# Performance work log

Measured on AMD Instinct MI355X. Metric: run time of the kernel, lower is better.

## Reference

```python
import jax, jax.numpy as jnp
import numpy as np

B, N, T, D, H = 4, 8, 512, 256, 8
DK = D // H


def _dwconv(x, w, b=None):
    # x: (BN, D, T) depthwise conv, kernel 3, padding 'same', groups=D
    y = jax.lax.conv_general_dilated(
        x, w, window_strides=(1,), padding='SAME',
        feature_group_count=x.shape[1],
        dimension_numbers=('NCH', 'OIH', 'NCH'))
    if b is not None:
        y = y + b[None, :, None]
    return y


def setup_inputs() -> dict:
    key = jax.random.key(0)
    ks = jax.random.split(key, 16)
    s = 1.0 / np.sqrt(D)
    s3 = 1.0 / np.sqrt(3 * D)
    inp = {
        'query': jax.random.normal(ks[0], (B, N, T, D), jnp.float32),
        'key': jax.random.normal(ks[1], (B, N, T, D), jnp.float32),
        'value': jax.random.normal(ks[2], (B, N, T, D), jnp.float32),
        'key_padding_mask': jax.random.randint(ks[3], (B, N, T), 0, 2, jnp.int32),
        # depthwise conv params
        'w_pos': jax.random.uniform(ks[4], (D, 1, 3), jnp.float32, -0.577, 0.577),
        'b_pos': jax.random.uniform(ks[5], (D,), jnp.float32, -0.577, 0.577),
        # physics-initialized differential operators (still learnable floats)
        'w_vel': jnp.tile(jnp.array([-1.0, 0.0, 1.0], jnp.float32)[None, None, :], (D, 1, 1)),
        'w_acc': jnp.tile(jnp.array([1.0, -2.0, 1.0], jnp.float32)[None, None, :], (D, 1, 1)),
        # fusion / projection linears (stored as (in, out))
        'Wq': jax.random.uniform(ks[6], (3 * D, D), jnp.float32, -s3, s3),
        'bq': jax.random.uniform(ks[7], (D,), jnp.float32, -s3, s3),
        'Wk': jax.random.uniform(ks[8], (3 * D, D), jnp.float32, -s3, s3),
        'bk': jax.random.uniform(ks[9], (D,), jnp.float32, -s3, s3),
        'Wv': jax.random.uniform(ks[10], (D, D), jnp.float32, -s, s),
        'bv': jax.random.uniform(ks[11], (D,), jnp.float32, -s, s),
        'Wo': jax.random.uniform(ks[12], (D, D), jnp.float32, -s, s),
        'bo': jax.random.uniform(ks[13], (D,), jnp.float32, -s, s),
    }
    return inp


def reference(query, key, value, key_padding_mask,
              w_pos, b_pos, w_vel, w_acc,
              Wq, bq, Wk, bk, Wv, bv, Wo, bo):
    b, n, t, d = query.shape
    scale = jnp.float32(1.0 / np.sqrt(DK))

    def kin_feats(x):
        xin = x.reshape(b * n, t, d).transpose(0, 2, 1)  # (BN, D, T)
        p = _dwconv(xin, w_pos, b_pos)
        v = _dwconv(xin, w_vel)
        a = _dwconv(xin, w_acc)
        return jnp.concatenate([p, v, a], axis=1).transpose(0, 2, 1)  # (BN, T, 3D)

    qc = kin_feats(query)
    kc = kin_feats(key)

    Q = (qc @ Wq + bq).reshape(b, n, t, H, DK).transpose(0, 1, 3, 2, 4)  # (B,N,H,Tq,dk)
    K = (kc @ Wk + bk).reshape(b, n, t, H, DK).transpose(0, 1, 3, 2, 4)
    V = (value @ Wv + bv).reshape(b, n, t, H, DK).transpose(0, 1, 3, 2, 4)

    scores = jnp.einsum('bnhqd,bnhkd->bnhqk', Q, K) * scale
    mask = key_padding_mask.astype(bool)[:, :, None, None, :]  # (B,N,1,1,Tk)
    scores = jnp.where(mask, jnp.float32(-1e9), scores)
    attn = jax.nn.softmax(scores, axis=-1)  # dropout is identity in eval

    ctx = jnp.einsum('bnhqk,bnhkd->bnhqd', attn, V)
    ctx = ctx.transpose(0, 1, 3, 2, 4).reshape(b, n, t, d)
    return ctx @ Wo + bo
```

## Files before the change

kernel.cpp:

```cpp
#include <hip/hip_runtime.h>
#include <math.h>


typedef __attribute__((ext_vector_type(8))) short bf16x8;
typedef __attribute__((ext_vector_type(4))) float f32x4;
typedef __attribute__((ext_vector_type(16))) float f32x16;
typedef __attribute__((ext_vector_type(4))) int i32x4;

__device__ __forceinline__ unsigned short f2bf(float f) {
    unsigned u = __float_as_uint(f);
    return (unsigned short)((u + 0x7fff + ((u >> 16) & 1)) >> 16);
}
__device__ __forceinline__ float bf2f(unsigned short h) {
    return __uint_as_float(((unsigned)h) << 16);
}
__device__ __forceinline__ float ex2(float x) {
    float r; asm("v_exp_f32 %0, %1" : "=v"(r) : "v"(x)); return r;
}
__device__ __forceinline__ int cvtpk(float lo, float hi) {
    int r; asm("v_cvt_pk_bf16_f32 %0, %1, %2" : "=v"(r) : "v"(lo), "v"(hi)); return r;
}
__device__ __forceinline__ void gll16(const void* gsrc, const void* ldst) {
    __builtin_amdgcn_global_load_lds(
        (const __attribute__((address_space(1))) unsigned int*)gsrc,
        (__attribute__((address_space(3))) unsigned int*)ldst, 16, 0, 0);
}

#define SCL (0.17677669529663689f * 1.4426950408889634f)

#define OFF_XPQ  0u
#define OFF_XPK  8421376u
#define OFF_VB   16842752u
#define OFF_BTQ  25231360u
#define OFF_BTK  25624576u
#define OFF_BEFF 26017792u
#define OFF_WVT  26019840u
#define OFF_WOT  26150912u
#define OFF_QB   26413056u
#define OFF_KB   34801664u
#define OFF_VV   43190272u
#define OFF_CTX  51578880u

__global__ __launch_bounds__(256) void cvtprep(
    const float* __restrict__ q, const float* __restrict__ k, const float* __restrict__ v,
    unsigned short* __restrict__ xpq, unsigned short* __restrict__ xpk,
    unsigned short* __restrict__ vb,
    const float* __restrict__ Wq, const float* __restrict__ Wk,
    const float* __restrict__ bq, const float* __restrict__ bk,
    const float* __restrict__ wp, const float* __restrict__ wv,
    const float* __restrict__ wa, const float* __restrict__ b_pos,
    const float* __restrict__ Wv, const float* __restrict__ Wo,
    unsigned short* __restrict__ BtQ, unsigned short* __restrict__ BtK,
    float* __restrict__ beff, unsigned short* __restrict__ WVT,
    unsigned short* __restrict__ WOT)
{
    int bid = blockIdx.x;
    if (bid < 4112) {
        int idx = bid * 256 + threadIdx.x;
        int which = idx / 526336;
        int r = idx - which * 526336;
        int bn = r / 16448;
        int rr = r - bn * 16448;
        int p = rr >> 5;
        int c8 = (rr & 31) * 8;
        const float* src = which ? k : q;
        unsigned short* dst = which ? xpk : xpq;
        unsigned o[4] = {0, 0, 0, 0};
        if (p != 0 && p != 513) {
            const float* s = src + ((size_t)(bn * 512 + p - 1) * 256 + c8);
            float4 a = *(const float4*)s;
            float4 b = *(const float4*)(s + 4);
            o[0] = f2bf(a.x) | ((unsigned)f2bf(a.y) << 16);
            o[1] = f2bf(a.z) | ((unsigned)f2bf(a.w) << 16);
            o[2] = f2bf(b.x) | ((unsigned)f2bf(b.y) << 16);
            o[3] = f2bf(b.z) | ((unsigned)f2bf(b.w) << 16);
        }
        unsigned* d = (unsigned*)(dst + ((size_t)(bn * 514 + p) * 256 + c8));
        d[0] = o[0]; d[1] = o[1]; d[2] = o[2]; d[3] = o[3];
    } else if (bid < 6160) {
        int idx = (bid - 4112) * 256 + threadIdx.x;
        int row = idx >> 5;
        int c8 = (idx & 31) * 8;
        const float* s = v + ((size_t)row * 256 + c8);
        float4 a = *(const float4*)s;
        float4 b = *(const float4*)(s + 4);
        unsigned* d = (unsigned*)(vb + ((size_t)row * 256 + c8));
        d[0] = f2bf(a.x) | ((unsigned)f2bf(a.y) << 16);
        d[1] = f2bf(a.z) | ((unsigned)f2bf(a.w) << 16);
        d[2] = f2bf(b.x) | ((unsigned)f2bf(b.y) << 16);
        d[3] = f2bf(b.z) | ((unsigned)f2bf(b.w) << 16);
    } else if (bid < 7696) {
        int idx = (bid - 6160) * 256 + threadIdx.x;
        int which = idx / 196608;
        int r = idx - which * 196608;
        int j = r >> 16;
        int rem = r & 65535;
        int n = rem >> 8;
        int d = rem & 255;
        const float* W = which ? Wk : Wq;
        float val = wp[d * 3 + j] * W[d * 256 + n]
                  + wv[d * 3 + j] * W[(256 + d) * 256 + n]
                  + wa[d * 3 + j] * W[(512 + d) * 256 + n];
        if (!which) val *= SCL;
        (which ? BtK : BtQ)[n * 768 + j * 256 + d] = f2bf(val);
    } else if (bid < 8208) {
        int idx = (bid - 7696) * 256 + threadIdx.x;
        int which = idx >> 16;
        int r = idx & 65535;
        int n = r >> 8, kk = r & 255;
        if (!which) {
            WVT[n * 256 + kk] = f2bf(Wv[kk * 256 + n]);
        } else {
            float vv = Wo[kk * 256 + n];
            unsigned short hi = f2bf(vv);
            WOT[n * 512 + kk] = hi;
            WOT[n * 512 + 256 + kk] = f2bf(vv - bf2f(hi));
        }
    } else {
        int which = bid - 8208;
        int n = threadIdx.x;
        const float* W = which ? Wk : Wq;
        const float* bb = which ? bk : bq;
        float s = bb[n];
        for (int d = 0; d < 256; ++d) s = fmaf(b_pos[d], W[d * 256 + n], s);
        if (!which) s *= SCL;
        beff[which * 256 + n] = s;
    }
}

template<int KTOT, bool IM2COL, typename OutT>
__device__ __forceinline__ void gemm97(
    const unsigned short* __restrict__ A, const unsigned short* __restrict__ Bt,
    const float* __restrict__ bias, OutT* __restrict__ Out,
    unsigned short* As, unsigned short* Bs)
{
    const int tid = threadIdx.x;
    const int wid = tid >> 6, l = tid & 63;
    const int l31 = l & 31, h2 = l >> 5;
    const int wm = wid >> 1, wn = wid & 1;
    const int m0 = blockIdx.x * 128, n0 = blockIdx.y * 128;

    f32x16 acc[2][2] = {};

    for (int k0 = 0; k0 < KTOT; k0 += 64) {
        __syncthreads();
        #pragma unroll
        for (int q = 0; q < 4; ++q) {
            int cidx = q * 256 + wid * 64 + l;
            int row = cidx >> 3;
            int csrc = ((cidx & 7) ^ (row & 7)) * 8;
            const unsigned short* asrc;
            if constexpr (IM2COL) {
                int seq = m0 >> 9, t0 = m0 & 511;
                asrc = A + ((size_t)(seq * 514 + t0 + row + (k0 >> 8)) * 256 + (k0 & 255) + csrc);
            } else {
                asrc = A + ((size_t)(m0 + row) * 256 + (k0 & 255) + csrc);
            }
            gll16(asrc, As + (q * 256 + wid * 64) * 8);
            gll16(Bt + (size_t)(n0 + row) * KTOT + k0 + csrc, Bs + (q * 256 + wid * 64) * 8);
        }
        __syncthreads();
        #pragma unroll
        for (int ks = 0; ks < 4; ++ks) {
            bf16x8 af[2], bfr[2];
            #pragma unroll
            for (int mt = 0; mt < 2; ++mt) {
                int r = wm * 64 + mt * 32 + l31;
                af[mt] = *(const bf16x8*)&As[r * 64 + (((ks * 2 + h2) ^ (r & 7)) * 8)];
            }
            #pragma unroll
            for (int nt = 0; nt < 2; ++nt) {
                int rn = wn * 64 + nt * 32 + l31;
                bfr[nt] = *(const bf16x8*)&Bs[rn * 64 + (((ks * 2 + h2) ^ (rn & 7)) * 8)];
            }
            #pragma unroll
            for (int mt = 0; mt < 2; ++mt)
                #pragma unroll
                for (int nt = 0; nt < 2; ++nt)
                    acc[mt][nt] = __builtin_amdgcn_mfma_f32_32x32x16_bf16(af[mt], bfr[nt], acc[mt][nt], 0, 0, 0);
        }
    }

    #pragma unroll
    for (int nt = 0; nt < 2; ++nt) {
        const int col = n0 + wn * 64 + nt * 32 + l31;
        const float bb = bias[col];
        #pragma unroll
        for (int mt = 0; mt < 2; ++mt) {
            #pragma unroll
            for (int r = 0; r < 16; ++r) {
                const int row = m0 + wm * 64 + mt * 32 + 4 * h2 + (r & 3) + 8 * (r >> 2);
                float v = acc[mt][nt][r] + bb;
                if constexpr (sizeof(OutT) == 2) Out[(size_t)row * 256 + col] = (OutT)f2bf(v);
                else Out[(size_t)row * 256 + col] = v;
            }
        }
    }
}

__global__ __launch_bounds__(256) void proj_fused(
    const unsigned short* __restrict__ XPQ, const unsigned short* __restrict__ XPK,
    const unsigned short* __restrict__ VB,
    const unsigned short* __restrict__ BTQ, const unsigned short* __restrict__ BTK,
    const unsigned short* __restrict__ WVT,
    const float* __restrict__ BEFF, const float* __restrict__ bv,
    unsigned short* __restrict__ QB, unsigned short* __restrict__ KB,
    unsigned short* __restrict__ VV)
{
    __shared__ alignas(16) unsigned short As[8192];
    __shared__ alignas(16) unsigned short Bs[8192];
    const int z = blockIdx.z;
    if (z == 0)      gemm97<768, true, unsigned short>(XPQ, BTQ, BEFF, QB, As, Bs);
    else if (z == 1) gemm97<768, true, unsigned short>(XPK, BTK, BEFF + 256, KB, As, Bs);
    else             gemm97<256, false, unsigned short>(VB, WVT, bv, VV, As, Bs);
}

__global__ __launch_bounds__(256) void outproj(
    const unsigned short* __restrict__ CTX, const unsigned short* __restrict__ WOT,
    const float* __restrict__ bo, float* __restrict__ Out)
{
    __shared__ alignas(16) unsigned short As[8192];
    __shared__ alignas(16) unsigned short Bs[8192];
    gemm97<512, false, float>(CTX, WOT, bo, Out, As, Bs);
}

__global__ __launch_bounds__(256) void attn_mfma(const unsigned short* __restrict__ Qb,
                                                 const unsigned short* __restrict__ Kb,
                                                 const unsigned short* __restrict__ Vv,
                                                 const int* __restrict__ mask,
                                                 unsigned short* __restrict__ ctx) {
    __shared__ alignas(16) unsigned short Qs[64 * 32];
    __shared__ alignas(16) unsigned short Ks[2][128 * 32];
    __shared__ alignas(16) unsigned short VsT[2][32 * 136];
    __shared__ float Mb[2][128];

    const int qt = blockIdx.x, bnh = blockIdx.y;
    const int bn = bnh >> 3, h = bnh & 7;
    const int tid = threadIdx.x, wid = tid >> 6, l = tid & 63;
    const int g = l >> 4, r15 = l & 15;
    const unsigned short* Qg = Qb + (size_t)bn * 512 * 256 + h * 32;
    const unsigned short* Kg = Kb + (size_t)bn * 512 * 256 + h * 32;
    const unsigned short* Vg = Vv + (size_t)bn * 512 * 256 + h * 32;
    const int* mp = mask + bn * 512;

    auto stageK = [&](int k0, int b) {
        #pragma unroll
        for (int qq = 0; qq < 2; ++qq) {
            int cidx = qq * 256 + wid * 64 + l;
            int row = cidx >> 2, csrc = ((cidx & 3) ^ (row & 3)) * 8;
            gll16(Kg + ((size_t)(k0 + row)) * 256 + csrc, &Ks[b][qq * 2048 + wid * 512]);
        }
    };

    {
        int cidx = wid * 64 + l;
        gll16(Qg + ((size_t)(qt * 64 + (cidx >> 2))) * 256 + (cidx & 3) * 8, Qs + wid * 512);
    }
    stageK(0, 0);
    {
        #pragma unroll
        for (int qq = 0; qq < 2; ++qq) {
            int key = l + 64 * qq;
            i32x4 vr = *(const i32x4*)(const void*)(Vg + (size_t)key * 256 + wid * 8);
            #pragma unroll
            for (int i = 0; i < 4; ++i) {
                unsigned u = (unsigned)vr[i];
                VsT[0][(wid * 8 + 2 * i) * 136 + key] = (unsigned short)(u & 0xffff);
                VsT[0][(wid * 8 + 2 * i + 1) * 136 + key] = (unsigned short)(u >> 16);
            }
        }
        if (tid < 128) Mb[0][tid] = (mp[tid] != 0) ? -1e9f : 0.f;
    }
    __syncthreads();

    const bf16x8 bq = *(const bf16x8*)&Qs[(wid * 16 + r15) * 32 + g * 8];

    float mrun = -1e30f, lrun = 0.f;
    f32x4 accO[2] = {};

    for (int kt = 0; kt < 4; ++kt) {
        const int cur = kt & 1, nxt = cur ^ 1;
        const int k0n = kt * 128 + 128;

        i32x4 vr[2];
        int mraw = 0;
        if (kt < 3) {
            stageK(k0n, nxt);
            #pragma unroll
            for (int qq = 0; qq < 2; ++qq)
                vr[qq] = *(const i32x4*)(const void*)(Vg + ((size_t)(k0n + l + 64 * qq)) * 256 + wid * 8);
            if (tid < 128) mraw = mp[k0n + tid];
        }

        float p[8][4];
        float rmax = -3e38f;
        __builtin_amdgcn_s_setprio(1);
        #pragma unroll
        for (int t2 = 0; t2 < 8; ++t2) {
            const int base = 32 * (t2 >> 1) + 4 * (t2 & 1);
            const int arow = base + 8 * (r15 >> 2) + (r15 & 3);
            bf16x8 ak = *(const bf16x8*)&Ks[cur][arow * 32 + ((g ^ (arow & 3)) * 8)];
            f32x4 cin = *(const f32x4*)&Mb[cur][base + 8 * g];
            f32x4 st = __builtin_amdgcn_mfma_f32_16x16x32_bf16(ak, bq, cin, 0, 0, 0);
            #pragma unroll
            for (int r = 0; r < 4; ++r) p[t2][r] = st[r];
            rmax = fmaxf(rmax, fmaxf(fmaxf(st[0], st[1]), fmaxf(st[2], st[3])));
        }
        __builtin_amdgcn_s_setprio(0);
        rmax = fmaxf(rmax, __shfl_xor(rmax, 16, 64));
        rmax = fmaxf(rmax, __shfl_xor(rmax, 32, 64));

        if (__ballot(rmax > mrun)) {
            float mnew = fmaxf(mrun, rmax);
            float fs = ex2(mrun - mnew);
            lrun *= fs;
            accO[0] *= fs;
            accO[1] *= fs;
            mrun = mnew;
        }
        float psum = 0.f;
        #pragma unroll
        for (int t2 = 0; t2 < 8; ++t2)
            #pragma unroll
            for (int r = 0; r < 4; ++r) {
                float e = ex2(p[t2][r] - mrun);
                p[t2][r] = e;
                psum += e;
            }
        psum += __shfl_xor(psum, 16, 64);
        psum += __shfl_xor(psum, 32, 64);
        lrun += psum;

        bf16x8 pb[4];
        #pragma unroll
        for (int s = 0; s < 4; ++s) {
            i32x4 bi = {cvtpk(p[2 * s][0], p[2 * s][1]), cvtpk(p[2 * s][2], p[2 * s][3]),
                        cvtpk(p[2 * s + 1][0], p[2 * s + 1][1]), cvtpk(p[2 * s + 1][2], p[2 * s + 1][3])};
            pb[s] = __builtin_bit_cast(bf16x8, bi);
        }

        __builtin_amdgcn_s_setprio(1);
        #pragma unroll
        for (int mt = 0; mt < 2; ++mt)
            #pragma unroll
            for (int s = 0; s < 4; ++s) {
                bf16x8 av = *(const bf16x8*)&VsT[cur][(mt * 16 + r15) * 136 + 32 * s + 8 * g];
                accO[mt] = __builtin_amdgcn_mfma_f32_16x16x32_bf16(av, pb[s], accO[mt], 0, 0, 0);
            }
        __builtin_amdgcn_s_setprio(0);

        if (kt < 3) {
            #pragma unroll
            for (int qq = 0; qq < 2; ++qq) {
                int key = l + 64 * qq;
                #pragma unroll
                for (int i = 0; i < 4; ++i) {
                    unsigned u = (unsigned)vr[qq][i];
                    VsT[nxt][(wid * 8 + 2 * i) * 136 + key] = (unsigned short)(u & 0xffff);
                    VsT[nxt][(wid * 8 + 2 * i + 1) * 136 + key] = (unsigned short)(u >> 16);
                }
            }
            if (tid < 128) Mb[nxt][tid] = (mraw != 0) ? -1e9f : 0.f;
        }
        __syncthreads();
    }

    const float inv = 1.f / lrun;
    const size_t orow = (size_t)bn * 512 + qt * 64 + wid * 16 + r15;
    #pragma unroll
    for (int mt = 0; mt < 2; ++mt) {
        ushort4 o;
        o.x = f2bf(accO[mt][0] * inv);
        o.y = f2bf(accO[mt][1] * inv);
        o.z = f2bf(accO[mt][2] * inv);
        o.w = f2bf(accO[mt][3] * inv);
        *(ushort4*)&ctx[orow * 256 + h * 32 + mt * 16 + 4 * g] = o;
    }
}

extern "C" void kernel_launch(void* const* d_in, const int* in_sizes, int n_in,
                              void* d_out, int out_size, void* d_ws, size_t ws_size,
                              hipStream_t stream) {
    const float* query = (const float*)d_in[0];
    const float* key   = (const float*)d_in[1];
    const float* value = (const float*)d_in[2];
    const int*   kpm   = (const int*)d_in[3];
    const float* w_pos = (const float*)d_in[4];
    const float* b_pos = (const float*)d_in[5];
    const float* w_vel = (const float*)d_in[6];
    const float* w_acc = (const float*)d_in[7];
    const float* Wq    = (const float*)d_in[8];
    const float* bq    = (const float*)d_in[9];
    const float* Wk    = (const float*)d_in[10];
    const float* bk    = (const float*)d_in[11];
    const float* Wv    = (const float*)d_in[12];
    const float* bv    = (const float*)d_in[13];
    const float* Wo    = (const float*)d_in[14];
    const float* bo    = (const float*)d_in[15];

    unsigned char* w = (unsigned char*)d_ws;
    unsigned short* XPQ = (unsigned short*)(w + OFF_XPQ);
    unsigned short* XPK = (unsigned short*)(w + OFF_XPK);
    unsigned short* VB  = (unsigned short*)(w + OFF_VB);
    unsigned short* BTQ = (unsigned short*)(w + OFF_BTQ);
    unsigned short* BTK = (unsigned short*)(w + OFF_BTK);
    float*          BEFF= (float*)(w + OFF_BEFF);
    unsigned short* WVT = (unsigned short*)(w + OFF_WVT);
    unsigned short* WOT = (unsigned short*)(w + OFF_WOT);
    unsigned short* QB  = (unsigned short*)(w + OFF_QB);
    unsigned short* KB  = (unsigned short*)(w + OFF_KB);
    unsigned short* VV  = (unsigned short*)(w + OFF_VV);
    unsigned short* CTX = (unsigned short*)(w + OFF_CTX);

    cvtprep<<<8210, 256, 0, stream>>>(query, key, value, XPQ, XPK, VB,
                                      Wq, Wk, bq, bk, w_pos, w_vel, w_acc, b_pos,
                                      Wv, Wo, BTQ, BTK, BEFF, WVT, WOT);

    proj_fused<<<dim3(128, 2, 3), 256, 0, stream>>>(XPQ, XPK, VB, BTQ, BTK, WVT,
                                                    BEFF, bv, QB, KB, VV);

    attn_mfma<<<dim3(8, 256), 256, 0, stream>>>(QB, KB, VV, kpm, CTX);

    outproj<<<dim3(128, 2), 256, 0, stream>>>(CTX, WOT, bo, (float*)d_out);
}
```

Baseline: 95.38 us.

## Drop split-bf16 Wo and double attention query tile to 128 rows

The output projection weights are now stored as a single bf16 copy instead of a hi/lo split pair, which halves the K dimension of the out-projection GEMM. The attention kernel now runs 512 threads (8 waves) per block over 128 query rows, so each staged K/V tile serves twice as many queries and K/V global traffic falls. In exchange the out-projection loses the extra precision the split gave, and fewer but larger attention blocks may change occupancy.

```diff
diff --git a/kernel.cpp b/kernel.cpp
--- a/kernel.cpp
+++ b/kernel.cpp
@@ -10,9 +10,6 @@
 __device__ __forceinline__ unsigned short f2bf(float f) {
     unsigned u = __float_as_uint(f);
     return (unsigned short)((u + 0x7fff + ((u >> 16) & 1)) >> 16);
-}
-__device__ __forceinline__ float bf2f(unsigned short h) {
-    return __uint_as_float(((unsigned)h) << 16);
 }
 __device__ __forceinline__ float ex2(float x) {
     float r; asm("v_exp_f32 %0, %1" : "=v"(r) : "v"(x)); return r;
@@ -108,14 +105,8 @@
         int which = idx >> 16;
         int r = idx & 65535;
         int n = r >> 8, kk = r & 255;
-        if (!which) {
-            WVT[n * 256 + kk] = f2bf(Wv[kk * 256 + n]);
-        } else {
-            float vv = Wo[kk * 256 + n];
-            unsigned short hi = f2bf(vv);
-            WOT[n * 512 + kk] = hi;
-            WOT[n * 512 + 256 + kk] = f2bf(vv - bf2f(hi));
-        }
+        if (!which) WVT[n * 256 + kk] = f2bf(Wv[kk * 256 + n]);
+        else        WOT[n * 256 + kk] = f2bf(Wo[kk * 256 + n]);
     } else {
         int which = bid - 8208;
         int n = threadIdx.x;
@@ -221,15 +212,15 @@
 {
     __shared__ alignas(16) unsigned short As[8192];
     __shared__ alignas(16) unsigned short Bs[8192];
-    gemm97<512, false, float>(CTX, WOT, bo, Out, As, Bs);
-}
-
-__global__ __launch_bounds__(256) void attn_mfma(const unsigned short* __restrict__ Qb,
+    gemm97<256, false, float>(CTX, WOT, bo, Out, As, Bs);
+}
+
+__global__ __launch_bounds__(512) void attn_mfma(const unsigned short* __restrict__ Qb,
                                                  const unsigned short* __restrict__ Kb,
                                                  const unsigned short* __restrict__ Vv,
                                                  const int* __restrict__ mask,
                                                  unsigned short* __restrict__ ctx) {
-    __shared__ alignas(16) unsigned short Qs[64 * 32];
+    __shared__ alignas(16) unsigned short Qs[128 * 32];
     __shared__ alignas(16) unsigned short Ks[2][128 * 32];
     __shared__ alignas(16) unsigned short VsT[2][32 * 136];
     __shared__ float Mb[2][128];
@@ -242,32 +233,23 @@
     const unsigned short* Kg = Kb + (size_t)bn * 512 * 256 + h * 32;
     const unsigned short* Vg = Vv + (size_t)bn * 512 * 256 + h * 32;
     const int* mp = mask + bn * 512;
+    const int srow = tid >> 2;
+    const int vkey = tid & 127, vd0 = (tid >> 7) * 8;
 
     auto stageK = [&](int k0, int b) {
-        #pragma unroll
-        for (int qq = 0; qq < 2; ++qq) {
-            int cidx = qq * 256 + wid * 64 + l;
-            int row = cidx >> 2, csrc = ((cidx & 3) ^ (row & 3)) * 8;
-            gll16(Kg + ((size_t)(k0 + row)) * 256 + csrc, &Ks[b][qq * 2048 + wid * 512]);
-        }
+        int csrc = (((tid & 3) ^ (srow & 3))) * 8;
+        gll16(Kg + ((size_t)(k0 + srow)) * 256 + csrc, &Ks[b][wid * 512]);
     };
 
-    {
-        int cidx = wid * 64 + l;
-        gll16(Qg + ((size_t)(qt * 64 + (cidx >> 2))) * 256 + (cidx & 3) * 8, Qs + wid * 512);
-    }
+    gll16(Qg + ((size_t)(qt * 128 + srow)) * 256 + (tid & 3) * 8, Qs + wid * 512);
     stageK(0, 0);
     {
-        #pragma unroll
-        for (int qq = 0; qq < 2; ++qq) {
-            int key = l + 64 * qq;
-            i32x4 vr = *(const i32x4*)(const void*)(Vg + (size_t)key * 256 + wid * 8);
-            #pragma unroll
-            for (int i = 0; i < 4; ++i) {
-                unsigned u = (unsigned)vr[i];
-                VsT[0][(wid * 8 + 2 * i) * 136 + key] = (unsigned short)(u & 0xffff);
-                VsT[0][(wid * 8 + 2 * i + 1) * 136 + key] = (unsigned short)(u >> 16);
-            }
+        i32x4 vr = *(const i32x4*)(const void*)(Vg + (size_t)vkey * 256 + vd0);
+        #pragma unroll
+        for (int i = 0; i < 4; ++i) {
+            unsigned u = (unsigned)vr[i];
+            VsT[0][(vd0 + 2 * i) * 136 + vkey] = (unsigned short)(u & 0xffff);
+            VsT[0][(vd0 + 2 * i + 1) * 136 + vkey] = (unsigned short)(u >> 16);
         }
         if (tid < 128) Mb[0][tid] = (mp[tid] != 0) ? -1e9f : 0.f;
     }
@@ -282,13 +264,11 @@
         const int cur = kt & 1, nxt = cur ^ 1;
         const int k0n = kt * 128 + 128;
 
-        i32x4 vr[2];
+        i32x4 vr;
         int mraw = 0;
         if (kt < 3) {
             stageK(k0n, nxt);
-            #pragma unroll
-            for (int qq = 0; qq < 2; ++qq)
-                vr[qq] = *(const i32x4*)(const void*)(Vg + ((size_t)(k0n + l + 64 * qq)) * 256 + wid * 8);
+            vr = *(const i32x4*)(const void*)(Vg + ((size_t)(k0n + vkey)) * 256 + vd0);
             if (tid < 128) mraw = mp[k0n + tid];
         }
 
@@ -351,14 +331,10 @@
 
         if (kt < 3) {
             #pragma unroll
-            for (int qq = 0; qq < 2; ++qq) {
-                int key = l + 64 * qq;
-                #pragma unroll
-                for (int i = 0; i < 4; ++i) {
-                    unsigned u = (unsigned)vr[qq][i];
-                    VsT[nxt][(wid * 8 + 2 * i) * 136 + key] = (unsigned short)(u & 0xffff);
-                    VsT[nxt][(wid * 8 + 2 * i + 1) * 136 + key] = (unsigned short)(u >> 16);
-                }
+            for (int i = 0; i < 4; ++i) {
+                unsigned u = (unsigned)vr[i];
+                VsT[nxt][(vd0 + 2 * i) * 136 + vkey] = (unsigned short)(u & 0xffff);
+                VsT[nxt][(vd0 + 2 * i + 1) * 136 + vkey] = (unsigned short)(u >> 16);
             }
             if (tid < 128) Mb[nxt][tid] = (mraw != 0) ? -1e9f : 0.f;
         }
@@ -366,7 +342,7 @@
     }
 
     const float inv = 1.f / lrun;
-    const size_t orow = (size_t)bn * 512 + qt * 64 + wid * 16 + r15;
+    const size_t orow = (size_t)bn * 512 + qt * 128 + wid * 16 + r15;
     #pragma unroll
     for (int mt = 0; mt < 2; ++mt) {
         ushort4 o;
@@ -419,7 +395,7 @@
     proj_fused<<<dim3(128, 2, 3), 256, 0, stream>>>(XPQ, XPK, VB, BTQ, BTK, WVT,
                                                     BEFF, bv, QB, KB, VV);
 
-    attn_mfma<<<dim3(8, 256), 256, 0, stream>>>(QB, KB, VV, kpm, CTX);
+    attn_mfma<<<dim3(4, 256), 512, 0, stream>>>(QB, KB, VV, kpm, CTX);
 
     outproj<<<dim3(128, 2), 256, 0, stream>>>(CTX, WOT, bo, (float*)d_out);
 }
```

Measured after the change: 91.90 us. 3.6% less time.
